# Kernel tuning notes

Measured on AMD Instinct MI355X. Metric: run time of the kernel, lower is better.

The kernel has to match this reference:

```python
import jax, jax.numpy as jnp
import numpy as np

B, T, D, H, E, K = 4, 1024, 1024, 16, 8, 2
HS = D // H
DFF = 4 * D
N = B * T
CAP_MAX = N * K // E  # static upper bound on expert capacity (all tokens non-skip)
SKIP_THR = 0.5
LN_EPS = 1e-5


def _ln(x, g, b):
    m = x.mean(-1, keepdims=True)
    v = x.var(-1, keepdims=True)  # biased, matches torch LayerNorm
    return (x - m) * jax.lax.rsqrt(v + LN_EPS) * g + b


def setup_inputs() -> dict:
    key = jax.random.key(0)
    ks = jax.random.split(key, 20)
    s = 0.02
    nrm = lambda k, shp: jax.random.normal(k, shp, dtype=jnp.float32) * s
    return {
        "x": jax.random.normal(ks[0], (B, T, D), dtype=jnp.float32),
        "noise": jax.random.normal(ks[1], (B, T, E), dtype=jnp.float32),
        "ln1_g": jnp.ones((D,), jnp.float32), "ln1_b": jnp.zeros((D,), jnp.float32),
        "wq": nrm(ks[2], (D, D)), "wk": nrm(ks[3], (D, D)), "wv": nrm(ks[4], (D, D)),
        "w_proj": nrm(ks[5], (D, D)), "b_proj": jnp.zeros((D,), jnp.float32),
        "ln2_g": jnp.ones((D,), jnp.float32), "ln2_b": jnp.zeros((D,), jnp.float32),
        "w_router": nrm(ks[6], (D, E)), "b_router": jnp.zeros((E,), jnp.float32),
        "w_noise": nrm(ks[7], (D, E)), "b_noise": jnp.zeros((E,), jnp.float32),
        "w_skip": nrm(ks[8], (D, 1)), "b_skip": jnp.zeros((1,), jnp.float32),
        "ew1": nrm(ks[9], (E, D, DFF)), "eb1": jnp.zeros((E, DFF), jnp.float32),
        "ew2": nrm(ks[10], (E, DFF, D)), "eb2": jnp.zeros((E, D), jnp.float32),
    }


def _block(x, noise, ln1_g, ln1_b, wq, wk, wv, w_proj, b_proj, ln2_g, ln2_b,
           w_router, b_router, w_noise, b_noise, w_skip, b_skip, ew1, eb1, ew2, eb2):
    # ---- multi-head causal self-attention (dropout is identity in eval) ----
    h = _ln(x, ln1_g, ln1_b)
    q = (h @ wq).reshape(B, T, H, HS)
    k = (h @ wk).reshape(B, T, H, HS)
    v = (h @ wv).reshape(B, T, H, HS)
    # NOTE: original scales by C**-0.5 with C = n_embed (not head_size)
    wei = jnp.einsum("bqhd,bkhd->bhqk", q, k) * (D ** -0.5)
    tril = jnp.tril(jnp.ones((T, T), bool))
    wei = jnp.where(tril, wei, -jnp.inf)
    wei = jax.nn.softmax(wei, axis=-1)
    attn = jnp.einsum("bhqk,bkhd->bqhd", wei, v).reshape(B, T, D)
    x1 = x + attn @ w_proj + b_proj

    # ---- cross-layer sparse MoE with skip routing ----
    h2 = _ln(x1, ln2_g, ln2_b)
    logits = h2 @ w_router + b_router                      # [B,T,E]
    noisy = logits + noise * jax.nn.softplus(h2 @ w_noise + b_noise)
    vals, idx = jax.lax.top_k(noisy, K)                    # [B,T,K]
    sparse = jnp.full_like(noisy, -jnp.inf)
    bi = jnp.arange(B)[:, None, None]
    ti = jnp.arange(T)[None, :, None]
    sparse = sparse.at[bi, ti, idx].set(vals)
    gates = jax.nn.softmax(sparse, axis=-1)                # [B,T,E]
    skip = (jax.nn.sigmoid(h2 @ w_skip + b_skip)[..., 0] > SKIP_THR)  # [B,T]

    fx = h2.reshape(N, D)
    fg = gates.reshape(N, E)
    fi = idx.reshape(N, K)
    nsk = ~skip.reshape(N)                                  # non-skip tokens
    n_ns = nsk.sum()
    capacity = (n_ns * K) // E                              # floor(tokens*K/E * 1.0)

    # per-expert dispatch with first-come capacity truncation (flat-token order)
    mask = (fi[None, :, :] == jnp.arange(E)[:, None, None]).any(-1) & nsk[None, :]  # [E,N]
    rank = jnp.cumsum(mask, axis=1) - 1                     # arrival order among non-skip
    within = mask & (rank < capacity)
    slot = jnp.where(within, rank, CAP_MAX)
    buf = jnp.full((E, CAP_MAX + 1), N, dtype=jnp.int32)
    buf = buf.at[jnp.arange(E)[:, None], slot].set(jnp.arange(N, dtype=jnp.int32)[None, :])
    tok = buf[:, :CAP_MAX]                                  # [E,CAP_MAX] token id or N (pad)
    valid = tok < N

    xp = jnp.concatenate([fx, jnp.zeros((1, D), fx.dtype)], axis=0)
    xin = xp[tok]                                           # [E,CAP_MAX,D]
    mid = jax.nn.relu(jnp.einsum("ecd,edf->ecf", xin, ew1) + eb1[:, None, :])
    yout = jnp.einsum("ecf,efd->ecd", mid, ew2) + eb2[:, None, :]
    gp = jnp.concatenate([fg, jnp.zeros((1, E), fg.dtype)], axis=0)
    gsel = gp[tok, jnp.arange(E)[:, None]]                  # [E,CAP_MAX]
    wout = yout * (gsel * valid)[..., None]

    updates = jnp.zeros((N + 1, D), fx.dtype).at[tok.reshape(-1)].add(wout.reshape(-1, D))[:N]
    moe_out = jnp.where(nsk[:, None], updates, fx).reshape(B, T, D)  # skipped tokens pass ln2(x1) through
    return x1 + moe_out


def reference(x, noise, ln1_g, ln1_b, wq, wk, wv, w_proj, b_proj, ln2_g, ln2_b,
              w_router, b_router, w_noise, b_noise, w_skip, b_skip, ew1, eb1, ew2, eb2):
    return _block(x, noise, ln1_g, ln1_b, wq, wk, wv, w_proj, b_proj, ln2_g, ln2_b,
                  w_router, b_router, w_noise, b_noise, w_skip, b_skip, ew1, eb1, ew2, eb2)
```

## Files before the change

### kernel.cpp

```cpp
#include <hip/hip_runtime.h>
#include <math.h>

#define TOK_N   4096
#define DMODEL  1024
#define NEXP    8
#define DFFD    4096
#define CAPMAX  1024

typedef __bf16 bf16x8 __attribute__((ext_vector_type(8)));
typedef __bf16 bf16x4 __attribute__((ext_vector_type(4)));
typedef float  f32x4  __attribute__((ext_vector_type(4)));

__device__ __forceinline__ f32x4 MFMA16(bf16x8 a, bf16x8 b, f32x4 c){
  return __builtin_amdgcn_mfma_f32_16x16x32_bf16(a, b, c, 0, 0, 0);
}

__device__ __forceinline__ void gl16(const __bf16* g, __bf16* l){
  __builtin_amdgcn_global_load_lds(
      (const __attribute__((address_space(1))) unsigned int*)g,
      (__attribute__((address_space(3))) unsigned int*)l, 16, 0, 0);
}

__device__ __forceinline__ float wave_sum(float x){
  #pragma unroll
  for (int o=32;o;o>>=1) x += __shfl_down(x,o);
  return x;
}

__global__ __launch_bounds__(256) void prep_kernel(
    const float* __restrict__ wq, const float* __restrict__ wk,
    const float* __restrict__ wv, const float* __restrict__ wp,
    __bf16* __restrict__ dh, __bf16* __restrict__ dl,
    const float* __restrict__ x, const float* __restrict__ g1,
    const float* __restrict__ b1, __bf16* __restrict__ hh, __bf16* __restrict__ hl)
{
  __shared__ float smem[64*65];
  int b = blockIdx.x, t = threadIdx.x;
  if (b < 1024){
    int z = b >> 8, rem = b & 255;
    int k0 = (rem >> 4) * 64, n0 = (rem & 15) * 64;
    const float* in = z==0?wq: z==1?wk: z==2?wv: wp;
    __bf16* oh = dh + (size_t)z*DMODEL*DMODEL;
    __bf16* ol = dl + (size_t)z*DMODEL*DMODEL;
    float (*tile)[65] = (float(*)[65])smem;
    #pragma unroll
    for (int i=0;i<4;i++){
      int row = (t>>4) + i*16, col = (t&15)*4;
      f32x4 f = __builtin_nontemporal_load((const f32x4*)&in[(size_t)(k0+row)*DMODEL + n0 + col]);
      tile[row][col]=f[0]; tile[row][col+1]=f[1]; tile[row][col+2]=f[2]; tile[row][col+3]=f[3];
    }
    __syncthreads();
    #pragma unroll
    for (int i=0;i<2;i++){
      int c = t + i*256;
      int orow = c>>3, kg = (c&7)*8;
      bf16x8 hv, lv;
      #pragma unroll
      for (int u=0;u<8;u++){
        float xv = tile[kg+u][orow];
        __bf16 hb = (__bf16)xv;
        hv[u]=hb; lv[u]=(__bf16)(xv-(float)hb);
      }
      *(bf16x8*)&oh[(size_t)(n0+orow)*DMODEL + k0 + kg] = hv;
      *(bf16x8*)&ol[(size_t)(n0+orow)*DMODEL + k0 + kg] = lv;
    }
  } else {
    int n = b - 1024;
    float4 v = ((const float4*)(x + (size_t)n*DMODEL))[t];
    float s  = v.x+v.y+v.z+v.w;
    float sq = v.x*v.x+v.y*v.y+v.z*v.z+v.w*v.w;
    s = wave_sum(s); sq = wave_sum(sq);
    int lane = t & 63, wid = t >> 6;
    if (lane==0){ smem[wid]=s; smem[8+wid]=sq; }
    __syncthreads();
    if (t==0){
      float a = smem[0]+smem[1]+smem[2]+smem[3];
      float c = smem[8]+smem[9]+smem[10]+smem[11];
      float mean = a*(1.0f/DMODEL);
      float var  = c*(1.0f/DMODEL) - mean*mean;
      smem[16] = mean; smem[17] = 1.0f/sqrtf(var + 1e-5f);
    }
    __syncthreads();
    float mean = smem[16], rstd = smem[17];
    float4 g4 = ((const float4*)g1)[t];
    float4 b4 = ((const float4*)b1)[t];
    float o_[4];
    o_[0] = (v.x-mean)*rstd*g4.x + b4.x;
    o_[1] = (v.y-mean)*rstd*g4.y + b4.y;
    o_[2] = (v.z-mean)*rstd*g4.z + b4.z;
    o_[3] = (v.w-mean)*rstd*g4.w + b4.w;
    bf16x4 h4, l4;
    #pragma unroll
    for (int i=0;i<4;i++){ __bf16 hb=(__bf16)o_[i]; h4[i]=hb; l4[i]=(__bf16)(o_[i]-(float)hb); }
    *(bf16x4*)&hh[(size_t)n*DMODEL + t*4] = h4;
    *(bf16x4*)&hl[(size_t)n*DMODEL + t*4] = l4;
  }
}

__global__ __launch_bounds__(256) void ln_router_kernel(
    const float* __restrict__ p0, const float* __restrict__ p1,
    const float* __restrict__ xres, const float* __restrict__ bproj,
    const float* __restrict__ g, const float* __restrict__ b,
    __bf16* __restrict__ oh, __bf16* __restrict__ ol, float* __restrict__ out,
    const float* __restrict__ wr, const float* __restrict__ br,
    const float* __restrict__ wn, const float* __restrict__ bn,
    const float* __restrict__ wsk, const float* __restrict__ bsk,
    const float* __restrict__ noise,
    int* __restrict__ idx2, float* __restrict__ gate2, int* __restrict__ nskv)
{
  int n = blockIdx.x, t = threadIdx.x;
  size_t ro = (size_t)n*DMODEL/4 + t;
  float4 a  = ((const float4*)p0)[ro];
  float4 a1 = ((const float4*)p1)[ro];
  float4 xr = ((const float4*)xres)[ro];
  float4 bp = ((const float4*)bproj)[t];
  float4 v;
  v.x = a.x+a1.x+xr.x+bp.x; v.y = a.y+a1.y+xr.y+bp.y;
  v.z = a.z+a1.z+xr.z+bp.z; v.w = a.w+a1.w+xr.w+bp.w;
  float s  = v.x+v.y+v.z+v.w;
  float sq = v.x*v.x+v.y*v.y+v.z*v.z+v.w*v.w;
  s = wave_sum(s); sq = wave_sum(sq);
  __shared__ float r1[4], r2[4];
  __shared__ float mean_s, rstd_s, sk_s;
  int lane = t & 63, wid = t >> 6;
  if (lane==0){ r1[wid]=s; r2[wid]=sq; }
  __syncthreads();
  if (t==0){
    float aa = r1[0]+r1[1]+r1[2]+r1[3];
    float cc = r2[0]+r2[1]+r2[2]+r2[3];
    float mean = aa*(1.0f/DMODEL);
    float var  = cc*(1.0f/DMODEL) - mean*mean;
    mean_s = mean; rstd_s = 1.0f/sqrtf(var + 1e-5f);
  }
  __syncthreads();
  float mean = mean_s, rstd = rstd_s;
  float4 g4 = ((const float4*)g)[t];
  float4 b4 = ((const float4*)b)[t];
  float o_[4];
  o_[0] = (v.x-mean)*rstd*g4.x + b4.x;
  o_[1] = (v.y-mean)*rstd*g4.y + b4.y;
  o_[2] = (v.z-mean)*rstd*g4.z + b4.z;
  o_[3] = (v.w-mean)*rstd*g4.w + b4.w;
  bf16x4 h4, l4;
  #pragma unroll
  for (int i=0;i<4;i++){ __bf16 hb=(__bf16)o_[i]; h4[i]=hb; l4[i]=(__bf16)(o_[i]-(float)hb); }
  *(bf16x4*)&oh[(size_t)n*DMODEL + t*4] = h4;
  *(bf16x4*)&ol[(size_t)n*DMODEL + t*4] = l4;
  int d0 = t*4;
  const float* wrp = wr + (size_t)d0*NEXP;
  const float* wnp = wn + (size_t)d0*NEXP;
  const float* wsp = wsk + d0;
  float vals[17];
  #pragma unroll
  for (int i=0;i<17;i++) vals[i]=0.f;
  #pragma unroll
  for (int i=0;i<4;i++){
    #pragma unroll
    for (int e=0;e<NEXP;e++){
      vals[e]   += o_[i]*wrp[i*NEXP+e];
      vals[8+e] += o_[i]*wnp[i*NEXP+e];
    }
    vals[16] += o_[i]*wsp[i];
  }
  __shared__ float red[4][17];
  #pragma unroll
  for (int i=0;i<17;i++){
    float xx = wave_sum(vals[i]);
    if (lane==0) red[wid][i] = xx;
  }
  __syncthreads();
  if (t==0){
    float noisy[NEXP];
    #pragma unroll
    for (int e=0;e<NEXP;e++){
      float lr = red[0][e]+red[1][e]+red[2][e]+red[3][e] + br[e];
      float pn = red[0][8+e]+red[1][8+e]+red[2][8+e]+red[3][8+e] + bn[e];
      float sp = fmaxf(pn,0.f) + log1pf(expf(-fabsf(pn)));
      noisy[e] = lr + noise[(size_t)n*NEXP + e]*sp;
    }
    float sk = red[0][16]+red[1][16]+red[2][16]+red[3][16] + bsk[0];
    sk_s = sk;
    nskv[n] = (sk <= 0.f) ? 1 : 0;
    int i0=0; float v0=noisy[0];
    #pragma unroll
    for (int e=1;e<NEXP;e++) if (noisy[e] > v0){ v0=noisy[e]; i0=e; }
    int i1=-1; float v1=-INFINITY;
    #pragma unroll
    for (int e=0;e<NEXP;e++) if (e!=i0 && noisy[e] > v1){ v1=noisy[e]; i1=e; }
    float tt = expf(v1 - v0);
    idx2[n*2+0]=i0; idx2[n*2+1]=i1;
    gate2[n*2+0]=1.0f/(1.0f+tt); gate2[n*2+1]=tt/(1.0f+tt);
  }
  __syncthreads();
  if (sk_s > 0.f){
    v.x += o_[0]; v.y += o_[1]; v.z += o_[2]; v.w += o_[3];
  }
  ((float4*)out)[ro] = v;
}

__global__ __launch_bounds__(256) void tconv_group(
    const float* __restrict__ ew1, const float* __restrict__ ew2,
    __bf16* __restrict__ e1T, __bf16* __restrict__ e2T, int e0, int G)
{
  __shared__ float tile[64][65];
  int z = blockIdx.z, t = threadIdx.x;
  const float* in; __bf16* out; int K, N, k0, n0;
  if (z < G){
    in = ew1 + (size_t)(e0+z)*DMODEL*DFFD; out = e1T + (size_t)z*DFFD*DMODEL;
    K = DMODEL; N = DFFD; k0 = blockIdx.y*64; n0 = blockIdx.x*64;
  } else {
    in = ew2 + (size_t)(e0+z-G)*DFFD*DMODEL; out = e2T + (size_t)(z-G)*DMODEL*DFFD;
    K = DFFD; N = DMODEL; k0 = blockIdx.x*64; n0 = blockIdx.y*64;
  }
  #pragma unroll
  for (int i=0;i<4;i++){
    int row = (t>>4) + i*16, col = (t&15)*4;
    f32x4 f = __builtin_nontemporal_load((const f32x4*)&in[(size_t)(k0+row)*N + n0 + col]);
    tile[row][col]=f[0]; tile[row][col+1]=f[1]; tile[row][col+2]=f[2]; tile[row][col+3]=f[3];
  }
  __syncthreads();
  #pragma unroll
  for (int i=0;i<2;i++){
    int c = t + i*256;
    int orow = c>>3, kg = (c&7)*8;
    bf16x8 hv;
    #pragma unroll
    for (int u=0;u<8;u++) hv[u] = (__bf16)tile[kg+u][orow];
    __builtin_nontemporal_store(hv, (bf16x8*)&out[(size_t)(n0+orow)*K + k0 + kg]);
  }
}

__global__ __launch_bounds__(256) void btrans_kernel(
    const __bf16* __restrict__ ih, const __bf16* __restrict__ il, int istride, int icol0,
    __bf16* __restrict__ oh, __bf16* __restrict__ ol){
  __shared__ __bf16 th[64][72], tl[64][72];
  int r0 = blockIdx.x*64, c0 = blockIdx.y*64;
  int t = threadIdx.x;
  {
    int r = t>>2, cg = (t&3)*16;
    size_t go = (size_t)(r0+r)*istride + icol0 + c0 + cg;
    *(bf16x8*)&th[r][cg]   = *(const bf16x8*)&ih[go];
    *(bf16x8*)&th[r][cg+8] = *(const bf16x8*)&ih[go+8];
    *(bf16x8*)&tl[r][cg]   = *(const bf16x8*)&il[go];
    *(bf16x8*)&tl[r][cg+8] = *(const bf16x8*)&il[go+8];
  }
  __syncthreads();
  {
    int c = t>>2, rg = (t&3)*16;
    bf16x8 a,b,e,f;
    #pragma unroll
    for (int u=0;u<8;u++){ a[u]=th[rg+u][c]; b[u]=th[rg+8+u][c]; e[u]=tl[rg+u][c]; f[u]=tl[rg+8+u][c]; }
    size_t go = (size_t)(c0+c)*TOK_N + r0 + rg;
    *(bf16x8*)&oh[go]   = a;
    *(bf16x8*)&oh[go+8] = b;
    *(bf16x8*)&ol[go]   = e;
    *(bf16x8*)&ol[go+8] = f;
  }
}

template<int MODE, bool SPLIT>
__global__ __launch_bounds__(256) void mgemm(
    const __bf16* __restrict__ Ah, const __bf16* __restrict__ Al, int Astride,
    const __bf16* __restrict__ Bh, const __bf16* __restrict__ Bl, int Bstride,
    const float* __restrict__ bias,
    float* __restrict__ Cf, __bf16* __restrict__ Ch, __bf16* __restrict__ Cl,
    int N, int K,
    const int* __restrict__ tok, const __bf16* __restrict__ zbuf)
{
  constexpr int BM = SPLIT ? 256 : 128;
  constexpr int AJ = BM/64;
  constexpr int MT = BM/32;
  if constexpr (MODE==2){
    int z = blockIdx.z;
    Bh  += (size_t)z*((size_t)DFFD*DMODEL);
    bias+= (size_t)z*DFFD;
    Ch  += (size_t)z*((size_t)CAPMAX*DFFD);
    tok += z*CAPMAX;
  }
  if constexpr (MODE==4){
    int ge = blockIdx.z>>2, kz = blockIdx.z&3;
    Ah  += (size_t)ge*((size_t)CAPMAX*DFFD) + kz*1024;
    Bh  += (size_t)ge*((size_t)DMODEL*DFFD) + kz*1024;
    Cf  += (size_t)blockIdx.z*((size_t)CAPMAX*DMODEL);
    tok += ge*CAPMAX;
  }
  if constexpr (MODE==5){
    int kz = blockIdx.z;
    Ah += kz*512; Al += kz*512; Bh += kz*512; Bl += kz*512;
    Cf += (size_t)kz*((size_t)TOK_N*DMODEL);
  }
  int m0 = blockIdx.y*BM, n0 = blockIdx.x*128;
  if ((MODE==2||MODE==4) && tok[m0] >= TOK_N) return;
  __shared__ __align__(16) __bf16 sAh[2*BM*32], sBh[2*128*32];
  __shared__ __align__(16) __bf16 sAl[SPLIT?2*BM*32:8], sBl[SPLIT?2*128*32:8];
  int t = threadIdx.x, lane = t&63, w = t>>6;
  int wr = w>>1, wc = w&1, fr = lane&15, kb = lane>>4;

  const __bf16* aB[AJ]; const __bf16* aBl[AJ]; bool aval[AJ];
  const __bf16* bB[2]; const __bf16* bBl[2];
  #pragma unroll
  for (int j=0;j<AJ;j++){
    int c = j*256 + w*64 + lane;
    int row = c>>2, grp = c&3;
    int sg = grp ^ ((row>>1)&3);
    if (MODE==2){
      int token = tok[m0+row];
      if (token < TOK_N){ aB[j] = Ah + (size_t)token*Astride + sg*8; aval[j]=true; }
      else              { aB[j] = zbuf + sg*8;                       aval[j]=false; }
    } else {
      aB[j] = Ah + (size_t)(m0+row)*Astride + sg*8; aval[j]=true;
      if (SPLIT) aBl[j] = Al + (size_t)(m0+row)*Astride + sg*8;
    }
  }
  #pragma unroll
  for (int j=0;j<2;j++){
    int c = j*256 + w*64 + lane;
    int row = c>>2, grp = c&3;
    int sg = grp ^ ((row>>1)&3);
    bB[j] = Bh + (size_t)(n0+row)*Bstride + sg*8;
    if (SPLIT) bBl[j] = Bl + (size_t)(n0+row)*Bstride + sg*8;
  }

  auto stage = [&](int buf, int kt){
    int baseA = buf*(BM*32);
    int baseB = buf*(128*32);
    #pragma unroll
    for (int j=0;j<AJ;j++){
      int cb8 = baseA + (j*256 + w*64)*8;
      gl16(aB[j] + (aval[j]? kt : 0), &sAh[cb8]);
      if constexpr (SPLIT) gl16(aBl[j] + kt, &sAl[cb8]);
    }
    #pragma unroll
    for (int j=0;j<2;j++){
      int cb8 = baseB + (j*256 + w*64)*8;
      gl16(bB[j] + kt, &sBh[cb8]);
      if constexpr (SPLIT) gl16(bBl[j] + kt, &sBl[cb8]);
    }
  };

  f32x4 acc[MT][4];
  #pragma unroll
  for (int mt=0;mt<MT;mt++)
    #pragma unroll
    for (int nt=0;nt<4;nt++) acc[mt][nt] = (f32x4){0.f,0.f,0.f,0.f};

  int nk = K >> 5;
  stage(0, 0);
  stage(1, 32);
  int xk = (kb ^ ((fr>>1)&3))*8;
  for (int ik=0; ik<nk; ik++){
    int cur = ik & 1;
    if (ik+1 < nk){
      if constexpr (SPLIT) asm volatile("s_waitcnt vmcnt(12)" ::: "memory");
      else                 asm volatile("s_waitcnt vmcnt(4)" ::: "memory");
    } else {
      asm volatile("s_waitcnt vmcnt(0)" ::: "memory");
    }
    __builtin_amdgcn_s_barrier();
    int fbA = cur*(BM*32);
    int fbB = cur*(128*32);
    bf16x8 aFh[MT], bFh[4];
    bf16x8 aFl[SPLIT?MT:1], bFl[SPLIT?4:1];
    #pragma unroll
    for (int mt=0;mt<MT;mt++) aFh[mt] = *(const bf16x8*)&sAh[fbA + (wr*(BM/2)+mt*16+fr)*32 + xk];
    #pragma unroll
    for (int nt=0;nt<4;nt++) bFh[nt] = *(const bf16x8*)&sBh[fbB + (wc*64+nt*16+fr)*32 + xk];
    if constexpr (SPLIT){
      #pragma unroll
      for (int mt=0;mt<MT;mt++) aFl[mt] = *(const bf16x8*)&sAl[fbA + (wr*(BM/2)+mt*16+fr)*32 + xk];
      #pragma unroll
      for (int nt=0;nt<4;nt++) bFl[nt] = *(const bf16x8*)&sBl[fbB + (wc*64+nt*16+fr)*32 + xk];
    }
    asm volatile("s_waitcnt lgkmcnt(0)" ::: "memory");
    __builtin_amdgcn_sched_barrier(0);
    __builtin_amdgcn_s_barrier();
    if (ik+2 < nk) stage(cur, (ik+2)<<5);
    __builtin_amdgcn_s_setprio(1);
    #pragma unroll
    for (int mt=0;mt<MT;mt++)
      #pragma unroll
      for (int nt=0;nt<4;nt++)
        acc[mt][nt] = MFMA16(aFh[mt], bFh[nt], acc[mt][nt]);
    if constexpr (SPLIT){
      #pragma unroll
      for (int mt=0;mt<MT;mt++)
        #pragma unroll
        for (int nt=0;nt<4;nt++){
          acc[mt][nt] = MFMA16(aFh[mt], bFl[nt], acc[mt][nt]);
          acc[mt][nt] = MFMA16(aFl[mt], bFh[nt], acc[mt][nt]);
        }
    }
    __builtin_amdgcn_s_setprio(0);
  }

  #pragma unroll
  for (int mt=0; mt<MT; mt++){
    int r0 = m0 + wr*(BM/2) + mt*16 + (lane>>4)*4;
    #pragma unroll
    for (int nt=0; nt<4; nt++){
      int col = n0 + wc*64 + nt*16 + fr;
      f32x4 v = acc[mt][nt];
      if constexpr (MODE==0){
        #pragma unroll
        for (int jj=0;jj<4;jj++){
          float val = v[jj];
          __bf16 hb = (__bf16)val;
          size_t idx = (size_t)(r0+jj)*N + col;
          Ch[idx] = hb; Cl[idx] = (__bf16)(val-(float)hb);
        }
      } else if constexpr (MODE==2){
        float bs = bias[col];
        #pragma unroll
        for (int jj=0;jj<4;jj++)
          Ch[(size_t)(r0+jj)*N + col] = (__bf16)fmaxf(v[jj]+bs, 0.f);
      } else {
        #pragma unroll
        for (int jj=0;jj<4;jj++)
          Cf[(size_t)(r0+jj)*N + col] = v[jj];
      }
    }
  }
}

__global__ __launch_bounds__(256) void gather_kernel(const float* __restrict__ yk,
    const int* __restrict__ tsrc, const float* __restrict__ gselb,
    const float* __restrict__ eb2, int e0, int G, float* __restrict__ out)
{
  int n = blockIdx.x, t = threadIdx.x;
  int s0 = tsrc[n*2], s1 = tsrc[n*2+1];
  float4 o; bool any = false;
  #pragma unroll
  for (int kk=0; kk<2; kk++){
    int src = kk ? s1 : s0;
    if (src < 0) continue;
    int e = src >> 10;
    int ge = e - e0;
    if (ge < 0 || ge >= G) continue;
    int r = src & (CAPMAX-1);
    if (!any){ o = ((const float4*)(out + (size_t)n*DMODEL))[t]; any = true; }
    float g = gselb[src];
    float4 acc = ((const float4*)(eb2 + (size_t)e*DMODEL))[t];
    #pragma unroll
    for (int z=0; z<4; z++){
      float4 p = ((const float4*)(yk + ((size_t)(ge*4+z)*CAPMAX + r)*DMODEL))[t];
      acc.x+=p.x; acc.y+=p.y; acc.z+=p.z; acc.w+=p.w;
    }
    o.x += g*acc.x; o.y += g*acc.y; o.z += g*acc.z; o.w += g*acc.w;
  }
  if (any) ((float4*)(out + (size_t)n*DMODEL))[t] = o;
}

__global__ __launch_bounds__(256) void attn_mfma_kernel(
    const __bf16* __restrict__ qkvh, const __bf16* __restrict__ qkvl,
    const __bf16* __restrict__ vth, const __bf16* __restrict__ vtl,
    __bf16* __restrict__ oh, __bf16* __restrict__ ol)
{
  __shared__ __align__(16) __bf16 Kh[2][64*64], Kl[2][64*64], Vh[2][64*64], Vl[2][64*64];
  __shared__ __align__(16) __bf16 Pt[2][4][16*64];
  int qtA = blockIdx.x, qtB = qtA + 8;
  int bh = blockIdx.y;
  int batch = bh>>4, head = bh&15;
  int t = threadIdx.x, lane = t&63, w = t>>6;
  int g = lane>>4, fr = lane&15;
  int col0 = head*64;
  size_t qbaseA = (size_t)(batch*1024 + qtA*64);
  size_t qbaseB = (size_t)(batch*1024 + qtB*64);
  const int QKS = 3*DMODEL;
  const float scale = 0.03125f;

  bf16x8 bQhA[2], bQlA[2], bQhB[2], bQlB[2];
  {
    int qrow = w*16 + fr;
    size_t rbA = (qbaseA+qrow)*QKS + col0 + g*8;
    size_t rbB = (qbaseB+qrow)*QKS + col0 + g*8;
    bQhA[0] = *(const bf16x8*)&qkvh[rbA];
    bQhA[1] = *(const bf16x8*)&qkvh[rbA+32];
    bQlA[0] = *(const bf16x8*)&qkvl[rbA];
    bQlA[1] = *(const bf16x8*)&qkvl[rbA+32];
    bQhB[0] = *(const bf16x8*)&qkvh[rbB];
    bQhB[1] = *(const bf16x8*)&qkvh[rbB+32];
    bQlB[0] = *(const bf16x8*)&qkvl[rbB];
    bQlB[1] = *(const bf16x8*)&qkvl[rbB+32];
  }

  auto stageKV = [&](int buf, int kt){
    size_t kbase = (size_t)(batch*1024 + kt*64);
    #pragma unroll
    for (int j=0;j<2;j++){
      int c = j*256 + t, row = c>>3, seg = c&7;
      int lb = (j*256 + w*64)*8;
      size_t gk = (kbase+row)*QKS + 1024 + col0 + ((seg^(row&7))*8);
      gl16(qkvh+gk, &Kh[buf][lb]);
      gl16(qkvl+gk, &Kl[buf][lb]);
      size_t gv = (size_t)(col0+row)*TOK_N + kbase + ((seg^(row&7))*8);
      gl16(vth+gv, &Vh[buf][lb]);
      gl16(vtl+gv, &Vl[buf][lb]);
    }
  };

  float mA = -INFINITY, lA = 0.f, mB = -INFINITY, lB = 0.f;
  f32x4 oA[4], oB[4];
  #pragma unroll
  for (int nt=0;nt<4;nt++){ oA[nt]=(f32x4){0.f,0.f,0.f,0.f}; oB[nt]=(f32x4){0.f,0.f,0.f,0.f}; }

  auto qk = [&](int cur, bool diag, bf16x8* bQh, bf16x8* bQl, f32x4* s){
    int ntmax = diag ? (w+1) : 4;
    #pragma unroll
    for (int nt=0;nt<4;nt++) s[nt]=(f32x4){0.f,0.f,0.f,0.f};
    __builtin_amdgcn_s_setprio(1);
    #pragma unroll
    for (int ks=0; ks<2; ks++){
      #pragma unroll
      for (int nt=0; nt<4; nt++){
        if (nt < ntmax){
          int kvr = nt*16 + fr;
          int sc_ = (ks*4 + g) ^ (kvr&7);
          bf16x8 aKh = *(const bf16x8*)&Kh[cur][kvr*64 + sc_*8];
          bf16x8 aKl = *(const bf16x8*)&Kl[cur][kvr*64 + sc_*8];
          s[nt] = MFMA16(aKh, bQh[ks], s[nt]);
          s[nt] = MFMA16(aKl, bQh[ks], s[nt]);
          s[nt] = MFMA16(aKh, bQl[ks], s[nt]);
        }
      }
    }
    __builtin_amdgcn_s_setprio(0);
  };

  auto smpv = [&](int cur, bool diag, f32x4* s, float& m_, float& l_, f32x4* o_){
    int ntmax = diag ? (w+1) : 4;
    float sv[4][4];
    float mx = -INFINITY;
    int ql = w*16 + fr;
    #pragma unroll
    for (int nt=0;nt<4;nt++)
      #pragma unroll
      for (int j=0;j<4;j++){
        float xv = s[nt][j]*scale;
        if (nt >= ntmax || (diag && (nt*16 + g*4 + j) > ql)) xv = -INFINITY;
        sv[nt][j] = xv;
        mx = fmaxf(mx, xv);
      }
    mx = fmaxf(mx, __shfl_xor(mx,16));
    mx = fmaxf(mx, __shfl_xor(mx,32));
    float nm = fmaxf(m_, mx);
    float scf = __expf(m_ - nm);
    float ps = 0.f;
    #pragma unroll
    for (int nt=0;nt<4;nt++)
      #pragma unroll
      for (int j=0;j<4;j++){
        float p = __expf(sv[nt][j] - nm);
        sv[nt][j] = p;
        ps += p;
      }
    ps += __shfl_xor(ps,16);
    ps += __shfl_xor(ps,32);
    l_ = l_*scf + ps;
    m_ = nm;
    #pragma unroll
    for (int nt=0;nt<4;nt++) o_[nt] = o_[nt]*scf;
    #pragma unroll
    for (int nt=0;nt<4;nt++){
      bf16x4 hv, lv;
      #pragma unroll
      for (int j=0;j<4;j++){
        float pv = sv[nt][j];
        __bf16 hb = (__bf16)pv;
        hv[j] = hb; lv[j] = (__bf16)(pv-(float)hb);
      }
      int el = fr*64 + (((2*nt + (g>>1)) ^ (fr&7))*8) + (g&1)*4;
      *(bf16x4*)&Pt[0][w][el] = hv;
      *(bf16x4*)&Pt[1][w][el] = lv;
    }
    int ksmax = (diag && w < 2) ? 1 : 2;
    __builtin_amdgcn_s_setprio(1);
    #pragma unroll
    for (int ks=0; ks<2; ks++){
      if (ks < ksmax){
        int pc = (4*ks + g) ^ (fr&7);
        bf16x8 bPh = *(const bf16x8*)&Pt[0][w][fr*64 + pc*8];
        bf16x8 bPl = *(const bf16x8*)&Pt[1][w][fr*64 + pc*8];
        #pragma unroll
        for (int nt=0; nt<4; nt++){
          int vr = nt*16 + fr;
          int vc = (ks*4 + g) ^ (vr&7);
          bf16x8 aVh = *(const bf16x8*)&Vh[cur][vr*64 + vc*8];
          bf16x8 aVl = *(const bf16x8*)&Vl[cur][vr*64 + vc*8];
          o_[nt] = MFMA16(aVh, bPh, o_[nt]);
          o_[nt] = MFMA16(aVl, bPh, o_[nt]);
          o_[nt] = MFMA16(aVh, bPl, o_[nt]);
        }
      }
    }
    __builtin_amdgcn_s_setprio(0);
  };

  stageKV(0, 0);
  for (int kt=0; kt<=qtB; kt++){
    int cur = kt&1;
    __syncthreads();
    if (kt < qtB) stageKV(cur^1, kt+1);
    bool doA = (kt <= qtA);
    f32x4 sA[4], sB[4];
    if (doA) qk(cur, kt==qtA, bQhA, bQlA, sA);
    qk(cur, kt==qtB, bQhB, bQlB, sB);
    if (doA) smpv(cur, kt==qtA, sA, mA, lA, oA);
    smpv(cur, kt==qtB, sB, mB, lB, oB);
  }

  auto writeOut = [&](size_t qbase, float l_, f32x4* o_){
    float inv = 1.0f/l_;
    #pragma unroll
    for (int nt=0;nt<4;nt++){
      bf16x4 hv, lv;
      #pragma unroll
      for (int j=0;j<4;j++){
        float val = o_[nt][j]*inv;
        __bf16 hb = (__bf16)val;
        hv[j] = hb; lv[j] = (__bf16)(val-(float)hb);
      }
      int el = fr*64 + (((2*nt + (g>>1)) ^ (fr&7))*8) + (g&1)*4;
      *(bf16x4*)&Pt[0][w][el] = hv;
      *(bf16x4*)&Pt[1][w][el] = lv;
    }
    #pragma unroll
    for (int r=0;r<2;r++){
      int c = r*4 + g;
      int el = fr*64 + ((c ^ (fr&7))*8);
      bf16x8 vh = *(const bf16x8*)&Pt[0][w][el];
      bf16x8 vl = *(const bf16x8*)&Pt[1][w][el];
      size_t go = (qbase + w*16 + fr)*DMODEL + col0 + c*8;
      *(bf16x8*)&oh[go] = vh;
      *(bf16x8*)&ol[go] = vl;
    }
  };
  writeOut(qbaseA, lA, oA);
  writeOut(qbaseB, lB, oB);
}

__global__ __launch_bounds__(256) void scan_kernel(const int* __restrict__ idx2,
    const float* __restrict__ gate2, const int* __restrict__ nskv,
    int* __restrict__ tok, float* __restrict__ gsel, float* __restrict__ zbuf,
    int* __restrict__ tsrc)
{
  int t = threadIdx.x;
  for (int i=t; i<NEXP*CAPMAX; i+=256){ tok[i]=TOK_N; gsel[i]=0.f; }
  for (int i=t; i<2*TOK_N; i+=256) tsrc[i] = -1;
  for (int i=t; i<1024; i+=256) zbuf[i]=0.f;
  __shared__ int cnts[256][NEXP];
  __shared__ int nns_part[256];
  __shared__ int cap_s;
  int loc[NEXP];
  #pragma unroll
  for (int e=0;e<NEXP;e++) loc[e]=0;
  int nn=0, base = t*16;
  for (int u=0;u<16;u++){
    int n = base+u;
    if (nskv[n]){ nn++; loc[idx2[n*2]]++; loc[idx2[n*2+1]]++; }
  }
  #pragma unroll
  for (int e=0;e<NEXP;e++) cnts[t][e]=loc[e];
  nns_part[t]=nn;
  __syncthreads();
  if (t < NEXP){ int run=0; for (int i=0;i<256;i++){ int c=cnts[i][t]; cnts[i][t]=run; run+=c; } }
  if (t == NEXP){ int sum=0; for (int i=0;i<256;i++) sum+=nns_part[i]; cap_s = sum/4; }
  __syncthreads();
  int capacity = cap_s;
  int run[NEXP];
  #pragma unroll
  for (int e=0;e<NEXP;e++) run[e]=cnts[t][e];
  for (int u=0;u<16;u++){
    int n = base+u;
    if (!nskv[n]) continue;
    #pragma unroll
    for (int kk=0;kk<2;kk++){
      int e = idx2[n*2+kk];
      int r = run[e]++;
      if (r < capacity){
        tok[e*CAPMAX+r]=n; gsel[e*CAPMAX+r]=gate2[n*2+kk];
        tsrc[n*2+kk] = e*CAPMAX + r;
      }
    }
  }
}

extern "C" void kernel_launch(void* const* d_in, const int* in_sizes, int n_in,
                              void* d_out, int out_size, void* d_ws, size_t ws_size,
                              hipStream_t stream) {
  const float* x      = (const float*)d_in[0];
  const float* noise  = (const float*)d_in[1];
  const float* ln1_g  = (const float*)d_in[2];
  const float* ln1_b  = (const float*)d_in[3];
  const float* wq     = (const float*)d_in[4];
  const float* wk     = (const float*)d_in[5];
  const float* wv     = (const float*)d_in[6];
  const float* w_proj = (const float*)d_in[7];
  const float* b_proj = (const float*)d_in[8];
  const float* ln2_g  = (const float*)d_in[9];
  const float* ln2_b  = (const float*)d_in[10];
  const float* w_rout = (const float*)d_in[11];
  const float* b_rout = (const float*)d_in[12];
  const float* w_noi  = (const float*)d_in[13];
  const float* b_noi  = (const float*)d_in[14];
  const float* w_skip = (const float*)d_in[15];
  const float* b_skip = (const float*)d_in[16];
  const float* ew1    = (const float*)d_in[17];
  const float* eb1    = (const float*)d_in[18];
  const float* ew2    = (const float*)d_in[19];
  const float* eb2    = (const float*)d_in[20];
  float* out = (float*)d_out;

  char* ws = (char*)d_ws;
  const size_t MB = 1024*1024;
  __bf16* h_hi   = (__bf16*)(ws + 0*MB);
  __bf16* h_lo   = (__bf16*)(ws + 8*MB);
  __bf16* qkv_hi = (__bf16*)(ws + 16*MB);
  __bf16* qkv_lo = (__bf16*)(ws + 40*MB);
  __bf16* wAllT_h= (__bf16*)(ws + 64*MB);
  __bf16* wAllT_l= (__bf16*)(ws + 72*MB);
  __bf16* vt_hi  = (__bf16*)(ws + 81*MB);
  __bf16* vt_lo  = (__bf16*)(ws + 89*MB);
  float*  pP     = (float*) (ws + 16*MB);
  __bf16* ao_hi = h_hi, *ao_lo = h_lo;

  int G; size_t off_mid, off_yk, off_e1, off_e2, off_meta;
  if (ws_size >= (size_t)338*MB){
    G = 8;  off_mid = 16;  off_yk = 80;  off_e1 = 208; off_e2 = 272; off_meta = 336;
  } else if (ws_size >= (size_t)178*MB){
    G = 4;  off_mid = 16;  off_yk = 48;  off_e1 = 112; off_e2 = 144; off_meta = 176;
  } else {
    G = 2;  off_e1 = 16;  off_e2 = 32;  off_mid = 48;  off_yk = 64;  off_meta = 96;
  }
  __bf16* e1T = (__bf16*)(ws + off_e1*MB);
  __bf16* e2T = (__bf16*)(ws + off_e2*MB);
  __bf16* mid = (__bf16*)(ws + off_mid*MB);
  float*  yk  = (float*) (ws + off_yk*MB);
  char* meta = ws + off_meta*MB;
  int*   idx2  = (int*)  (meta);
  float* gate2 = (float*)(meta + 32*1024);
  int*   nskv  = (int*)  (meta + 64*1024);
  int*   tokb  = (int*)  (meta + 80*1024);
  float* gselb = (float*)(meta + 112*1024);
  float* zbuf  = (float*)(meta + 144*1024);
  int*   tsrc  = (int*)  (meta + 160*1024);

  dim3 blk(256);
  prep_kernel<<<5120, blk, 0, stream>>>(wq, wk, wv, w_proj, wAllT_h, wAllT_l,
                                        x, ln1_g, ln1_b, h_hi, h_lo);
  mgemm<0,true><<<dim3(24,16), blk, 0, stream>>>(h_hi, h_lo, DMODEL, wAllT_h, wAllT_l, DMODEL,
      nullptr, nullptr, qkv_hi, qkv_lo, 3*DMODEL, DMODEL, nullptr, nullptr);
  btrans_kernel<<<dim3(64,16), blk, 0, stream>>>(qkv_hi, qkv_lo, 3*DMODEL, 2048, vt_hi, vt_lo);
  attn_mfma_kernel<<<dim3(8,64), blk, 0, stream>>>(qkv_hi, qkv_lo, vt_hi, vt_lo, ao_hi, ao_lo);
  mgemm<5,true><<<dim3(8,16,2), blk, 0, stream>>>(ao_hi, ao_lo, DMODEL,
      wAllT_h + (size_t)3*DMODEL*DMODEL, wAllT_l + (size_t)3*DMODEL*DMODEL, DMODEL,
      nullptr, pP, nullptr, nullptr, DMODEL, 512, nullptr, nullptr);
  ln_router_kernel<<<TOK_N, blk, 0, stream>>>(pP, pP + (size_t)TOK_N*DMODEL, x, b_proj,
      ln2_g, ln2_b, h_hi, h_lo, out,
      w_rout, b_rout, w_noi, b_noi, w_skip, b_skip, noise, idx2, gate2, nskv);
  scan_kernel<<<1, blk, 0, stream>>>(idx2, gate2, nskv, tokb, gselb, zbuf, tsrc);
  int ngrp = NEXP / G;
  for (int grp=0; grp<ngrp; grp++){
    int e0 = grp*G;
    tconv_group<<<dim3(64,16,2*G), blk, 0, stream>>>(ew1, ew2, e1T, e2T, e0, G);
    mgemm<2,false><<<dim3(32,8,G), blk, 0, stream>>>(h_hi, nullptr, DMODEL,
        e1T, nullptr, DMODEL, eb1 + (size_t)e0*DFFD,
        nullptr, mid, nullptr, DFFD, DMODEL, tokb + e0*CAPMAX, (const __bf16*)zbuf);
    mgemm<4,false><<<dim3(8,8,4*G), blk, 0, stream>>>(mid, nullptr, DFFD,
        e2T, nullptr, DFFD, nullptr,
        yk, nullptr, nullptr, DMODEL, 1024, tokb + e0*CAPMAX, nullptr);
    gather_kernel<<<TOK_N, blk, 0, stream>>>(yk, tsrc, gselb, eb2, e0, G, out);
  }
}
```

Measured before the change: 530.7 us.

## Use 512-thread blocks and triple-buffered LDS pipeline in mgemm

The split-precision GEMM path now runs 512 threads (8 waves) per 256x128 tile, so each wave computes a 64x64 sub-tile instead of 128x64. The shared-memory staging moves from double to triple buffering, which lets the second barrier and lgkmcnt wait before issuing the next prefetch be dropped. The intent is to halve per-wave accumulator registers, raise latency hiding and remove one barrier per k-step. Costs: LDS use grows by half, and correctness now rests on the third buffer keeping the prefetch from overwriting data other waves are still reading.

```diff
diff --git a/kernel.cpp b/kernel.cpp
--- a/kernel.cpp
+++ b/kernel.cpp
@@ -259,7 +259,7 @@
 }
 
 template<int MODE, bool SPLIT>
-__global__ __launch_bounds__(256) void mgemm(
+__global__ __launch_bounds__(SPLIT?512:256) void mgemm(
     const __bf16* __restrict__ Ah, const __bf16* __restrict__ Al, int Astride,
     const __bf16* __restrict__ Bh, const __bf16* __restrict__ Bl, int Bstride,
     const float* __restrict__ bias,
@@ -267,9 +267,11 @@
     int N, int K,
     const int* __restrict__ tok, const __bf16* __restrict__ zbuf)
 {
+  constexpr int THREADS = SPLIT ? 512 : 256;
   constexpr int BM = SPLIT ? 256 : 128;
-  constexpr int AJ = BM/64;
-  constexpr int MT = BM/32;
+  constexpr int BN = 128;
+  constexpr int AJ = (BM*4)/THREADS;
+  constexpr int BJ = (BN*4)/THREADS;
   if constexpr (MODE==2){
     int z = blockIdx.z;
     Bh  += (size_t)z*((size_t)DFFD*DMODEL);
@@ -289,18 +291,18 @@
     Ah += kz*512; Al += kz*512; Bh += kz*512; Bl += kz*512;
     Cf += (size_t)kz*((size_t)TOK_N*DMODEL);
   }
-  int m0 = blockIdx.y*BM, n0 = blockIdx.x*128;
+  int m0 = blockIdx.y*BM, n0 = blockIdx.x*BN;
   if ((MODE==2||MODE==4) && tok[m0] >= TOK_N) return;
-  __shared__ __align__(16) __bf16 sAh[2*BM*32], sBh[2*128*32];
-  __shared__ __align__(16) __bf16 sAl[SPLIT?2*BM*32:8], sBl[SPLIT?2*128*32:8];
+  __shared__ __align__(16) __bf16 sAh[3*BM*32], sBh[3*BN*32];
+  __shared__ __align__(16) __bf16 sAl[SPLIT?3*BM*32:8], sBl[SPLIT?3*BN*32:8];
   int t = threadIdx.x, lane = t&63, w = t>>6;
   int wr = w>>1, wc = w&1, fr = lane&15, kb = lane>>4;
 
   const __bf16* aB[AJ]; const __bf16* aBl[AJ]; bool aval[AJ];
-  const __bf16* bB[2]; const __bf16* bBl[2];
+  const __bf16* bB[BJ]; const __bf16* bBl[BJ];
   #pragma unroll
   for (int j=0;j<AJ;j++){
-    int c = j*256 + w*64 + lane;
+    int c = j*THREADS + t;
     int row = c>>2, grp = c&3;
     int sg = grp ^ ((row>>1)&3);
     if (MODE==2){
@@ -313,8 +315,8 @@
     }
   }
   #pragma unroll
-  for (int j=0;j<2;j++){
-    int c = j*256 + w*64 + lane;
+  for (int j=0;j<BJ;j++){
+    int c = j*THREADS + t;
     int row = c>>2, grp = c&3;
     int sg = grp ^ ((row>>1)&3);
     bB[j] = Bh + (size_t)(n0+row)*Bstride + sg*8;
@@ -323,24 +325,24 @@
 
   auto stage = [&](int buf, int kt){
     int baseA = buf*(BM*32);
-    int baseB = buf*(128*32);
+    int baseB = buf*(BN*32);
     #pragma unroll
     for (int j=0;j<AJ;j++){
-      int cb8 = baseA + (j*256 + w*64)*8;
+      int cb8 = baseA + (j*THREADS + w*64)*8;
       gl16(aB[j] + (aval[j]? kt : 0), &sAh[cb8]);
       if constexpr (SPLIT) gl16(aBl[j] + kt, &sAl[cb8]);
     }
     #pragma unroll
-    for (int j=0;j<2;j++){
-      int cb8 = baseB + (j*256 + w*64)*8;
+    for (int j=0;j<BJ;j++){
+      int cb8 = baseB + (j*THREADS + w*64)*8;
       gl16(bB[j] + kt, &sBh[cb8]);
       if constexpr (SPLIT) gl16(bBl[j] + kt, &sBl[cb8]);
     }
   };
 
-  f32x4 acc[MT][4];
-  #pragma unroll
-  for (int mt=0;mt<MT;mt++)
+  f32x4 acc[4][4];
+  #pragma unroll
+  for (int mt=0;mt<4;mt++)
     #pragma unroll
     for (int nt=0;nt<4;nt++) acc[mt][nt] = (f32x4){0.f,0.f,0.f,0.f};
 
@@ -349,41 +351,38 @@
   stage(1, 32);
   int xk = (kb ^ ((fr>>1)&3))*8;
   for (int ik=0; ik<nk; ik++){
-    int cur = ik & 1;
+    int cur = ik % 3;
     if (ik+1 < nk){
-      if constexpr (SPLIT) asm volatile("s_waitcnt vmcnt(12)" ::: "memory");
+      if constexpr (SPLIT) asm volatile("s_waitcnt vmcnt(6)" ::: "memory");
       else                 asm volatile("s_waitcnt vmcnt(4)" ::: "memory");
     } else {
       asm volatile("s_waitcnt vmcnt(0)" ::: "memory");
     }
     __builtin_amdgcn_s_barrier();
     int fbA = cur*(BM*32);
-    int fbB = cur*(128*32);
-    bf16x8 aFh[MT], bFh[4];
-    bf16x8 aFl[SPLIT?MT:1], bFl[SPLIT?4:1];
-    #pragma unroll
-    for (int mt=0;mt<MT;mt++) aFh[mt] = *(const bf16x8*)&sAh[fbA + (wr*(BM/2)+mt*16+fr)*32 + xk];
+    int fbB = cur*(BN*32);
+    bf16x8 aFh[4], bFh[4];
+    bf16x8 aFl[SPLIT?4:1], bFl[SPLIT?4:1];
+    #pragma unroll
+    for (int mt=0;mt<4;mt++) aFh[mt] = *(const bf16x8*)&sAh[fbA + (wr*64+mt*16+fr)*32 + xk];
     #pragma unroll
     for (int nt=0;nt<4;nt++) bFh[nt] = *(const bf16x8*)&sBh[fbB + (wc*64+nt*16+fr)*32 + xk];
     if constexpr (SPLIT){
       #pragma unroll
-      for (int mt=0;mt<MT;mt++) aFl[mt] = *(const bf16x8*)&sAl[fbA + (wr*(BM/2)+mt*16+fr)*32 + xk];
+      for (int mt=0;mt<4;mt++) aFl[mt] = *(const bf16x8*)&sAl[fbA + (wr*64+mt*16+fr)*32 + xk];
       #pragma unroll
       for (int nt=0;nt<4;nt++) bFl[nt] = *(const bf16x8*)&sBl[fbB + (wc*64+nt*16+fr)*32 + xk];
     }
-    asm volatile("s_waitcnt lgkmcnt(0)" ::: "memory");
-    __builtin_amdgcn_sched_barrier(0);
-    __builtin_amdgcn_s_barrier();
-    if (ik+2 < nk) stage(cur, (ik+2)<<5);
+    if (ik+2 < nk) stage((ik+2)%3, (ik+2)<<5);
     __builtin_amdgcn_s_setprio(1);
     #pragma unroll
-    for (int mt=0;mt<MT;mt++)
+    for (int mt=0;mt<4;mt++)
       #pragma unroll
       for (int nt=0;nt<4;nt++)
         acc[mt][nt] = MFMA16(aFh[mt], bFh[nt], acc[mt][nt]);
     if constexpr (SPLIT){
       #pragma unroll
-      for (int mt=0;mt<MT;mt++)
+      for (int mt=0;mt<4;mt++)
         #pragma unroll
         for (int nt=0;nt<4;nt++){
           acc[mt][nt] = MFMA16(aFh[mt], bFl[nt], acc[mt][nt]);
@@ -394,8 +393,8 @@
   }
 
   #pragma unroll
-  for (int mt=0; mt<MT; mt++){
-    int r0 = m0 + wr*(BM/2) + mt*16 + (lane>>4)*4;
+  for (int mt=0; mt<4; mt++){
+    int r0 = m0 + wr*64 + mt*16 + (lane>>4)*4;
     #pragma unroll
     for (int nt=0; nt<4; nt++){
       int col = n0 + wc*64 + nt*16 + fr;
@@ -744,14 +743,14 @@
   float* zbuf  = (float*)(meta + 144*1024);
   int*   tsrc  = (int*)  (meta + 160*1024);
 
-  dim3 blk(256);
+  dim3 blk(256), blk512(512);
   prep_kernel<<<5120, blk, 0, stream>>>(wq, wk, wv, w_proj, wAllT_h, wAllT_l,
                                         x, ln1_g, ln1_b, h_hi, h_lo);
-  mgemm<0,true><<<dim3(24,16), blk, 0, stream>>>(h_hi, h_lo, DMODEL, wAllT_h, wAllT_l, DMODEL,
+  mgemm<0,true><<<dim3(24,16), blk512, 0, stream>>>(h_hi, h_lo, DMODEL, wAllT_h, wAllT_l, DMODEL,
       nullptr, nullptr, qkv_hi, qkv_lo, 3*DMODEL, DMODEL, nullptr, nullptr);
   btrans_kernel<<<dim3(64,16), blk, 0, stream>>>(qkv_hi, qkv_lo, 3*DMODEL, 2048, vt_hi, vt_lo);
   attn_mfma_kernel<<<dim3(8,64), blk, 0, stream>>>(qkv_hi, qkv_lo, vt_hi, vt_lo, ao_hi, ao_lo);
-  mgemm<5,true><<<dim3(8,16,2), blk, 0, stream>>>(ao_hi, ao_lo, DMODEL,
+  mgemm<5,true><<<dim3(8,16,2), blk512, 0, stream>>>(ao_hi, ao_lo, DMODEL,
       wAllT_h + (size_t)3*DMODEL*DMODEL, wAllT_l + (size_t)3*DMODEL*DMODEL, DMODEL,
       nullptr, pP, nullptr, nullptr, DMODEL, 512, nullptr, nullptr);
   ln_router_kernel<<<TOK_N, blk, 0, stream>>>(pP, pP + (size_t)TOK_N*DMODEL, x, b_proj,
```

Result: faster. 507.8 us (-4.3%).
